# Optimization experiments

Hardware: AMD Instinct MI355X
Metric: run time of the kernel (lower is better)

Reference implementation:

```python
import jax, jax.numpy as jnp
import numpy as np

N, DEG, F, H, O, B = 100000, 16, 128, 128, 128, 8192


def setup_inputs() -> dict:
    key = jax.random.key(0)
    k1, k2, k3, k4, k5 = jax.random.split(key, 5)
    features = jax.random.normal(k1, (N, F), dtype=jnp.float32)
    w1 = jax.random.normal(k2, (2 * F, H), dtype=jnp.float32)
    w2 = jax.random.normal(k3, (2 * H, O), dtype=jnp.float32)
    neighbor_idx = jax.random.randint(k4, (N, DEG), 0, N, dtype=jnp.int32)
    nodes = jax.random.randint(k5, (B,), 0, N, dtype=jnp.int32)
    return {"features": features, "w1": w1, "w2": w2,
            "neighbor_idx": neighbor_idx, "nodes": nodes}


def reference(features, w1, w2, neighbor_idx, nodes):
    # Layer 1 (computed for all nodes, vectorized): mean-aggregate neighbor
    # raw features, concat with self features, project with w1.
    neigh_feat = features[neighbor_idx]                 # [N, DEG, F] gather
    agg1 = neigh_feat.mean(axis=1)                      # [N, F]
    h1 = jnp.concatenate([features, agg1], axis=-1) @ w1  # [N, H]

    # Layer 2 (batch nodes): mean-aggregate neighbor layer-1 embeddings,
    # concat with self layer-1 embedding, project with w2.
    h1_self = h1[nodes]                                 # [B, H]
    h1_neigh = h1[neighbor_idx[nodes]].mean(axis=1)     # [B, H]
    out = jnp.concatenate([h1_self, h1_neigh], axis=-1) @ w2  # [B, O]
    return out
```

## Files before the change

### kernel.cpp

```cpp
#include <hip/hip_runtime.h>


#define N_NODES 100000
#define DEG     16
#define FDIM    128
#define HDIM    128
#define B_NODES 8192

typedef __attribute__((ext_vector_type(8))) short bf16x8;
typedef __attribute__((ext_vector_type(8))) unsigned short u16x8;
typedef __attribute__((ext_vector_type(4))) float f32x4;
typedef __attribute__((ext_vector_type(2))) float f32x2;

static __device__ __forceinline__ unsigned short f2bf(float f) {
    union { float f; unsigned u; } v; v.f = f;
    unsigned r = v.u + 0x7fff + ((v.u >> 16) & 1);
    return (unsigned short)(r >> 16);
}
static __device__ __forceinline__ float bf2f(unsigned short b) {
    union { unsigned u; float f; } v; v.u = ((unsigned)b) << 16;
    return v.f;
}

__global__ __launch_bounds__(256)
void prep(const float* __restrict__ feat, const float* __restrict__ w1,
          const float* __restrict__ w2, unsigned short* __restrict__ fb,
          unsigned char* __restrict__ f8,
          unsigned short* __restrict__ w1T, unsigned short* __restrict__ w2T) {
    if (blockIdx.x < 6250) {
        long e = ((long)blockIdx.x * 256 + threadIdx.x) * 8;
        float4 v0 = *(const float4*)(feat + e);
        float4 v1 = *(const float4*)(feat + e + 4);
        u16x8 ob;
        ob[0] = f2bf(v0.x); ob[1] = f2bf(v0.y); ob[2] = f2bf(v0.z); ob[3] = f2bf(v0.w);
        ob[4] = f2bf(v1.x); ob[5] = f2bf(v1.y); ob[6] = f2bf(v1.z); ob[7] = f2bf(v1.w);
        *(u16x8*)(fb + e) = ob;
        int p0 = 0, p1 = 0;
        p0 = __builtin_amdgcn_cvt_pk_fp8_f32(v0.x, v0.y, p0, false);
        p0 = __builtin_amdgcn_cvt_pk_fp8_f32(v0.z, v0.w, p0, true);
        p1 = __builtin_amdgcn_cvt_pk_fp8_f32(v1.x, v1.y, p1, false);
        p1 = __builtin_amdgcn_cvt_pk_fp8_f32(v1.z, v1.w, p1, true);
        uint2 o8; o8.x = (unsigned)p0; o8.y = (unsigned)p1;
        *(uint2*)(f8 + e) = o8;
    } else {
        int bid = blockIdx.x - 6250;
        const float* w = (bid < 8) ? w1 : w2;
        unsigned short* wT = (bid < 8) ? w1T : w2T;
        int kb = (bid & 7) * 32;
        int n = threadIdx.x & 127, dk = threadIdx.x >> 7;
#pragma unroll
        for (int i = 0; i < 16; ++i) {
            int k = kb + dk * 16 + i;
            wT[n * 256 + k] = f2bf(w[k * 128 + n]);
        }
    }
}

__global__ __launch_bounds__(64)
void k1_agg(const unsigned char* __restrict__ f8, const int* __restrict__ nbr,
            unsigned short* __restrict__ agg) {
    __shared__ unsigned char L[16][1024];
    const int lane = threadIdx.x;
    const int node = blockIdx.x * 8 + (lane >> 3);
    const int sub = lane & 7;
    const int* idx = nbr + node * DEG;
    int4 i0 = *(const int4*)(idx);
    int4 i1 = *(const int4*)(idx + 4);
    int4 i2 = *(const int4*)(idx + 8);
    int4 i3 = *(const int4*)(idx + 12);
    const int id[16] = {i0.x, i0.y, i0.z, i0.w, i1.x, i1.y, i1.z, i1.w,
                        i2.x, i2.y, i2.z, i2.w, i3.x, i3.y, i3.z, i3.w};
#pragma unroll
    for (int d = 0; d < DEG; ++d) {
        const unsigned char* src = f8 + (long)id[d] * 128 + sub * 16;
        __builtin_amdgcn_global_load_lds(
            (const __attribute__((address_space(1))) unsigned int*)src,
            (__attribute__((address_space(3))) unsigned int*)(&L[d][lane * 16]),
            16, 0, 0);
    }
    asm volatile("s_waitcnt vmcnt(0)" ::: "memory");

    f32x2 s2[8];
#pragma unroll
    for (int j = 0; j < 8; ++j) s2[j] = (f32x2){0.f, 0.f};
#pragma unroll
    for (int d = 0; d < DEG; ++d) {
        uint4 v = *(const uint4*)(&L[d][lane * 16]);
        s2[0] += __builtin_amdgcn_cvt_pk_f32_fp8((int)v.x, false);
        s2[1] += __builtin_amdgcn_cvt_pk_f32_fp8((int)v.x, true);
        s2[2] += __builtin_amdgcn_cvt_pk_f32_fp8((int)v.y, false);
        s2[3] += __builtin_amdgcn_cvt_pk_f32_fp8((int)v.y, true);
        s2[4] += __builtin_amdgcn_cvt_pk_f32_fp8((int)v.z, false);
        s2[5] += __builtin_amdgcn_cvt_pk_f32_fp8((int)v.z, true);
        s2[6] += __builtin_amdgcn_cvt_pk_f32_fp8((int)v.w, false);
        s2[7] += __builtin_amdgcn_cvt_pk_f32_fp8((int)v.w, true);
    }
    u16x8 o0, o1;
#pragma unroll
    for (int j = 0; j < 8; ++j) {
        o0[j] = f2bf(s2[j >> 1][j & 1] * 0.0625f);
        o1[j] = f2bf(s2[4 + (j >> 1)][j & 1] * 0.0625f);
    }
    unsigned short* dst = agg + (long)node * 128 + sub * 16;
    *(u16x8*)dst = o0;
    *(u16x8*)(dst + 8) = o1;
}

__global__ __launch_bounds__(256, 2)
void g1(const unsigned short* __restrict__ fb, const unsigned short* __restrict__ agg,
        const unsigned short* __restrict__ w1T, unsigned short* __restrict__ h1) {
    __shared__ unsigned short Wlds[64 * 512];
    const int t = threadIdx.x, wave = t >> 6, lane = t & 63;
    const int m16 = lane & 15, quad = lane >> 4;
    const long row0 = (long)blockIdx.x * 128 + wave * 32;

    bf16x8 a[8][2];
#pragma unroll
    for (int kc = 0; kc < 8; ++kc) {
        const unsigned short* As = (kc < 4) ? (fb + kc * 32) : (agg + (kc - 4) * 32);
        a[kc][0] = *(const bf16x8*)(As + (row0 + m16) * 128 + quad * 8);
        a[kc][1] = *(const bf16x8*)(As + (row0 + 16 + m16) * 128 + quad * 8);
    }

#pragma unroll
    for (int i = 0; i < 16; ++i) {
        int o16 = i * 256 + t;
        int chunk = o16 >> 6;
        int kc = chunk >> 3, nt = chunk & 7;
        int n = nt * 16 + (lane & 15);
        int k0 = kc * 32 + (lane >> 4) * 8;
        const unsigned short* src = w1T + n * 256 + k0;
        __builtin_amdgcn_global_load_lds(
            (const __attribute__((address_space(1))) unsigned int*)src,
            (__attribute__((address_space(3))) unsigned int*)
                (((char*)Wlds) + (long)o16 * 16),
            16, 0, 0);
    }
    __syncthreads();

    f32x4 acc[2][8] = {};
#pragma unroll
    for (int kc = 0; kc < 8; ++kc) {
#pragma unroll
        for (int nt = 0; nt < 8; ++nt) {
            bf16x8 bv = *(const bf16x8*)(Wlds + (kc * 8 + nt) * 512 + lane * 8);
            acc[0][nt] = __builtin_amdgcn_mfma_f32_16x16x32_bf16(a[kc][0], bv, acc[0][nt], 0, 0, 0);
            acc[1][nt] = __builtin_amdgcn_mfma_f32_16x16x32_bf16(a[kc][1], bv, acc[1][nt], 0, 0, 0);
        }
    }

#pragma unroll
    for (int mt = 0; mt < 2; ++mt)
#pragma unroll
        for (int reg = 0; reg < 4; ++reg) {
            long grow = row0 + mt * 16 + quad * 4 + reg;
            if (grow >= N_NODES) continue;
#pragma unroll
            for (int nt = 0; nt < 8; ++nt)
                h1[grow * HDIM + nt * 16 + m16] = f2bf(acc[mt][nt][reg]);
        }
}

__global__ __launch_bounds__(256)
void g2_fused(const unsigned short* __restrict__ h1, const unsigned short* __restrict__ w2T,
              const int* __restrict__ nbr, const int* __restrict__ nodes,
              float* __restrict__ out) {
    __shared__ unsigned short X2[64][264];
    const int t = threadIdx.x, wave = t >> 6, lane = t & 63;
    const int m16 = lane & 15, quad = lane >> 4;
    const int b0 = blockIdx.x * 64;
    const int colb = m16 * 8;

    for (int g = 0; g < 4; ++g) {
        int Ln = wave * 16 + g * 4 + quad;
        int node = nodes[b0 + Ln];
        *(u16x8*)(&X2[Ln][colb]) = *(const u16x8*)(h1 + node * HDIM + colb);
        const int* idx = nbr + node * DEG;
        float s[8] = {0.f, 0.f, 0.f, 0.f, 0.f, 0.f, 0.f, 0.f};
#pragma unroll
        for (int d = 0; d < DEG; ++d) {
            int nb = idx[d];
            u16x8 v = *(const u16x8*)(h1 + nb * HDIM + colb);
#pragma unroll
            for (int j = 0; j < 8; ++j) s[j] += bf2f(v[j]);
        }
        u16x8 o;
#pragma unroll
        for (int j = 0; j < 8; ++j) o[j] = f2bf(s[j] * 0.0625f);
        *(u16x8*)(&X2[Ln][128 + colb]) = o;
    }
    __syncthreads();

    f32x4 acc[8] = {};
#pragma unroll
    for (int kc = 0; kc < 8; ++kc) {
        bf16x8 a = *(const bf16x8*)(&X2[wave * 16 + m16][kc * 32 + quad * 8]);
#pragma unroll
        for (int nt = 0; nt < 8; ++nt) {
            bf16x8 b = *(const bf16x8*)(w2T + (nt * 16 + m16) * 256 + kc * 32 + quad * 8);
            acc[nt] = __builtin_amdgcn_mfma_f32_16x16x32_bf16(a, b, acc[nt], 0, 0, 0);
        }
    }

#pragma unroll
    for (int nt = 0; nt < 8; ++nt)
#pragma unroll
        for (int reg = 0; reg < 4; ++reg) {
            int row = b0 + wave * 16 + quad * 4 + reg;
            out[row * 128 + nt * 16 + m16] = acc[nt][reg];
        }
}

extern "C" void kernel_launch(void* const* d_in, const int* in_sizes, int n_in,
                              void* d_out, int out_size, void* d_ws, size_t ws_size,
                              hipStream_t stream) {
    const float* feat  = (const float*)d_in[0];
    const float* w1    = (const float*)d_in[1];
    const float* w2    = (const float*)d_in[2];
    const int*   nbr   = (const int*)d_in[3];
    const int*   nodes = (const int*)d_in[4];
    float* out = (float*)d_out;

    char* ws = (char*)d_ws;
    unsigned short* fb  = (unsigned short*)ws;
    unsigned char*  f8  = (unsigned char*)(ws + 25600000);
    unsigned short* agg = (unsigned short*)(ws + 38400000);
    unsigned short* h1  = (unsigned short*)(ws + 64000000);
    unsigned short* w1T = (unsigned short*)(ws + 89600000);
    unsigned short* w2T = (unsigned short*)(ws + 89665536);

    prep<<<6266, 256, 0, stream>>>(feat, w1, w2, fb, f8, w1T, w2T);
    k1_agg<<<12500, 64, 0, stream>>>(f8, nbr, agg);
    g1<<<(N_NODES + 127) / 128, 256, 0, stream>>>(fb, agg, w1T, h1);
    g2_fused<<<B_NODES / 64, 256, 0, stream>>>(h1, w2T, nbr, nodes, out);
}
```

Before: 170.8 us.

## Double-buffer A and W1 tiles in LDS per k-chunk in g1 GEMM

Restructures the g1 layer-1 GEMM so it no longer preloads all A fragments into registers and the whole W1 into 64KB of LDS. Each 32-wide k-chunk of A and W1 is now streamed into double-buffered LDS with global_load_lds, and the next chunk is prefetched while MFMAs run on the current one. The smaller LDS footprint and fewer registers allow raising launch bounds to 4 blocks per CU for more occupancy. In exchange it adds two barriers per k-step, and the A rows read past N on the last block rely on padded buffers.

Result: no change. 169.8 us (-0.6%).

```diff
diff --git a/kernel.cpp b/kernel.cpp
--- a/kernel.cpp
+++ b/kernel.cpp
@@ -106,46 +106,62 @@
     *(u16x8*)(dst + 8) = o1;
 }
 
-__global__ __launch_bounds__(256, 2)
+#define STAGE1(KC, BUF)                                                                   \
+    do {                                                                                  \
+        const int kc_ = (KC);                                                             \
+        const unsigned short* Asel_ =                                                     \
+            (kc_ < 4) ? (fb + kc_ * 32) : (agg + (kc_ - 4) * 32);                         \
+        _Pragma("unroll")                                                                 \
+        for (int j_ = 0; j_ < 2; ++j_) {                                                  \
+            int sub_ = j_ * 4 + wave;                                                     \
+            int rowA_ = (sub_ >> 1) * 32 + (sub_ & 1) * 16 + m16;                         \
+            const unsigned short* ga_ = Asel_ + (row0 + rowA_) * 128 + quad * 8;          \
+            __builtin_amdgcn_global_load_lds(                                             \
+                (const __attribute__((address_space(1))) unsigned int*)ga_,               \
+                (__attribute__((address_space(3))) unsigned int*)                         \
+                    (&As_[BUF][(j_ * 256 + t) * 8]), 16, 0, 0);                           \
+            int n_ = sub_ * 16 + m16;                                                     \
+            const unsigned short* gw_ = w1T + n_ * 256 + kc_ * 32 + quad * 8;             \
+            __builtin_amdgcn_global_load_lds(                                             \
+                (const __attribute__((address_space(1))) unsigned int*)gw_,               \
+                (__attribute__((address_space(3))) unsigned int*)                         \
+                    (&Ws_[BUF][(j_ * 256 + t) * 8]), 16, 0, 0);                           \
+        }                                                                                 \
+    } while (0)
+
+__global__ __launch_bounds__(256, 4)
 void g1(const unsigned short* __restrict__ fb, const unsigned short* __restrict__ agg,
         const unsigned short* __restrict__ w1T, unsigned short* __restrict__ h1) {
-    __shared__ unsigned short Wlds[64 * 512];
+    __shared__ unsigned short As_[2][4096];
+    __shared__ unsigned short Ws_[2][4096];
     const int t = threadIdx.x, wave = t >> 6, lane = t & 63;
     const int m16 = lane & 15, quad = lane >> 4;
-    const long row0 = (long)blockIdx.x * 128 + wave * 32;
-
-    bf16x8 a[8][2];
+    const long row0 = (long)blockIdx.x * 128;
+
+    f32x4 acc[2][8] = {};
+    STAGE1(0, 0);
 #pragma unroll
     for (int kc = 0; kc < 8; ++kc) {
-        const unsigned short* As = (kc < 4) ? (fb + kc * 32) : (agg + (kc - 4) * 32);
-        a[kc][0] = *(const bf16x8*)(As + (row0 + m16) * 128 + quad * 8);
-        a[kc][1] = *(const bf16x8*)(As + (row0 + 16 + m16) * 128 + quad * 8);
-    }
-
-#pragma unroll
-    for (int i = 0; i < 16; ++i) {
-        int o16 = i * 256 + t;
-        int chunk = o16 >> 6;
-        int kc = chunk >> 3, nt = chunk & 7;
-        int n = nt * 16 + (lane & 15);
-        int k0 = kc * 32 + (lane >> 4) * 8;
-        const unsigned short* src = w1T + n * 256 + k0;
-        __builtin_amdgcn_global_load_lds(
-            (const __attribute__((address_space(1))) unsigned int*)src,
-            (__attribute__((address_space(3))) unsigned int*)
-                (((char*)Wlds) + (long)o16 * 16),
-            16, 0, 0);
-    }
-    __syncthreads();
-
-    f32x4 acc[2][8] = {};
-#pragma unroll
-    for (int kc = 0; kc < 8; ++kc) {
+        __builtin_amdgcn_s_barrier();
+        __builtin_amdgcn_sched_barrier(0);
+        if (kc < 7) {
+            STAGE1(kc + 1, (kc + 1) & 1);
+            asm volatile("s_waitcnt vmcnt(4)" ::: "memory");
+        } else {
+            asm volatile("s_waitcnt vmcnt(0)" ::: "memory");
+        }
+        __builtin_amdgcn_s_barrier();
+        __builtin_amdgcn_sched_barrier(0);
+
+        const unsigned short* Ab = As_[kc & 1];
+        const unsigned short* Wb = Ws_[kc & 1];
+        bf16x8 a0 = *(const bf16x8*)(Ab + (wave * 2 + 0) * 512 + lane * 8);
+        bf16x8 a1 = *(const bf16x8*)(Ab + (wave * 2 + 1) * 512 + lane * 8);
 #pragma unroll
         for (int nt = 0; nt < 8; ++nt) {
-            bf16x8 bv = *(const bf16x8*)(Wlds + (kc * 8 + nt) * 512 + lane * 8);
-            acc[0][nt] = __builtin_amdgcn_mfma_f32_16x16x32_bf16(a[kc][0], bv, acc[0][nt], 0, 0, 0);
-            acc[1][nt] = __builtin_amdgcn_mfma_f32_16x16x32_bf16(a[kc][1], bv, acc[1][nt], 0, 0, 0);
+            bf16x8 bv = *(const bf16x8*)(Wb + nt * 512 + lane * 8);
+            acc[0][nt] = __builtin_amdgcn_mfma_f32_16x16x32_bf16(a0, bv, acc[0][nt], 0, 0, 0);
+            acc[1][nt] = __builtin_amdgcn_mfma_f32_16x16x32_bf16(a1, bv, acc[1][nt], 0, 0, 0);
         }
     }
 
@@ -153,7 +169,7 @@
     for (int mt = 0; mt < 2; ++mt)
 #pragma unroll
         for (int reg = 0; reg < 4; ++reg) {
-            long grow = row0 + mt * 16 + quad * 4 + reg;
+            long grow = row0 + wave * 32 + mt * 16 + quad * 4 + reg;
             if (grow >= N_NODES) continue;
 #pragma unroll
             for (int nt = 0; nt < 8; ++nt)
```
